# Performance work log

Hardware: AMD Instinct MI355X
Metric: run time of the kernel (lower is better)

Reference implementation:

```python
import jax, jax.numpy as jnp
import numpy as np

NHEAD = 8  # matches init_kwargs

M_NODES = 20000
D_MODEL = 512
N_EDGES = 640000


def setup_inputs() -> dict:
    key = jax.random.key(0)
    ks = jax.random.split(key, 8)
    sc = 1.0 / np.sqrt(D_MODEL)
    return {
        "s": jax.random.normal(ks[0], (M_NODES, D_MODEL), dtype=jnp.float32),
        "edge_index": jax.random.randint(ks[1], (2, N_EDGES), 0, M_NODES, dtype=jnp.int64),
        "Wq": jax.random.normal(ks[2], (D_MODEL, D_MODEL), dtype=jnp.float32) * sc,
        "bq": jax.random.normal(ks[3], (D_MODEL,), dtype=jnp.float32) * sc,
        "Wkv": jax.random.normal(ks[4], (2 * D_MODEL, D_MODEL), dtype=jnp.float32) * sc,
        "bkv": jax.random.normal(ks[5], (2 * D_MODEL,), dtype=jnp.float32) * sc,
        "Wo": jax.random.normal(ks[6], (D_MODEL, D_MODEL), dtype=jnp.float32) * sc,
        "bo": jax.random.normal(ks[7], (D_MODEL,), dtype=jnp.float32) * sc,
    }


def reference(s, edge_index, Wq, bq, Wkv, bkv, Wo, bo):
    M, C = s.shape
    H = NHEAD
    Dh = C // H
    scale = 1.0 / np.sqrt(Dh).astype(np.float32)

    q = (s @ Wq.T + bq).reshape(M, H, Dh)            # [M,H,Dh]
    kv = (s @ Wkv.T + bkv).reshape(M, H, 2 * Dh)     # [M,H,2Dh]
    k, v = kv[..., :Dh], kv[..., Dh:]

    src, tgt = edge_index[0], edge_index[1]

    # per-edge attention logits [E,H]
    a = jnp.einsum('ehc,ehc->eh', q[tgt], k[src]) * scale

    # segment softmax over edges sharing the same target node
    a_max = jax.ops.segment_max(a, tgt, num_segments=M)        # [M,H]
    ex = jnp.exp(a - a_max[tgt])                               # [E,H]
    denom = jax.ops.segment_sum(ex, tgt, num_segments=M)      # [M,H]
    attn = ex / denom[tgt]                                     # [E,H]

    # weighted message aggregation: scatter-sum over target nodes
    o_msg = attn[..., None] * v[src]                           # [E,H,Dh]
    o = jax.ops.segment_sum(o_msg, tgt, num_segments=M)       # [M,H,Dh]
    o = o.reshape(M, C)
    return o @ Wo.T + bo
```

## Files before the change

### kernel.cpp

```cpp
#include <hip/hip_runtime.h>
#include <cmath>

#define MN 20000
#define DM 512
#define NE 640000
#define CAP 128
#define NT 20
#define TSHIFT 10

typedef short  bf16x8 __attribute__((ext_vector_type(8)));
typedef float  f32x4  __attribute__((ext_vector_type(4)));

__device__ __forceinline__ ushort f2b(float x) {
    unsigned u = __builtin_bit_cast(unsigned, x);
    u += 0x7FFF + ((u >> 16) & 1);
    return (ushort)(u >> 16);
}
__device__ __forceinline__ float b2f(ushort b) {
    return __builtin_bit_cast(float, (unsigned)b << 16);
}

#define NS4   (MN * DM / 4)
#define NWC4  (1536 * 512 / 4)
#define NWO4  (512 * 512 / 4)
#define NB4   (1536 / 4)

__device__ __forceinline__ const float* wc_src_row(int r, const float* Wq, const float* Wkv) {
    if (r < 512) return Wq + ((size_t)r << 9);
    if (r < 1024) { int h = (r - 512) >> 6, j = (r - 512) & 63;  return Wkv + ((size_t)(h * 128 + j) << 9); }
    { int h = (r - 1024) >> 6, j = (r - 1024) & 63; return Wkv + ((size_t)(h * 128 + 64 + j) << 9); }
}

__global__ void conv_all_k(const float* __restrict__ s, const float* __restrict__ Wq,
                           const float* __restrict__ Wkv, const float* __restrict__ Wo,
                           const float* __restrict__ bq, const float* __restrict__ bkv,
                           const int* __restrict__ esrc, const int* __restrict__ etgt,
                           int* __restrict__ counts, int* __restrict__ counts2,
                           ushort* __restrict__ s_b, ushort* __restrict__ Wc_b,
                           ushort* __restrict__ Wo_b, float* __restrict__ bc)
{
    int i = blockIdx.x * blockDim.x + threadIdx.x;
    if (i < NE) {
        int t = etgt[i];
        atomicAdd(&counts[t], 1);
        atomicAdd(&counts2[t * NT + (esrc[i] >> TSHIFT)], 1);
    }
    if (i < NS4) {
        float4 v = ((const float4*)s)[i];
        ushort4 o = { f2b(v.x), f2b(v.y), f2b(v.z), f2b(v.w) };
        ((ushort4*)s_b)[i] = o;
        return;
    }
    i -= NS4;
    if (i < NWC4) {
        int e = i * 4, row = e >> 9, col = e & 511;
        float4 v = *(const float4*)(wc_src_row(row, Wq, Wkv) + col);
        ushort4 o = { f2b(v.x), f2b(v.y), f2b(v.z), f2b(v.w) };
        ((ushort4*)Wc_b)[i] = o;
        return;
    }
    i -= NWC4;
    if (i < NWO4) {
        float4 v = ((const float4*)Wo)[i];
        ushort4 o = { f2b(v.x), f2b(v.y), f2b(v.z), f2b(v.w) };
        ((ushort4*)Wo_b)[i] = o;
        return;
    }
    i -= NWO4;
    if (i < NB4) {
#pragma unroll
        for (int u = 0; u < 4; ++u) {
            int r = i * 4 + u;
            float v;
            if (r < 512) v = bq[r];
            else if (r < 1024) { int h = (r - 512) >> 6, j = (r - 512) & 63;  v = bkv[h * 128 + j]; }
            else               { int h = (r - 1024) >> 6, j = (r - 1024) & 63; v = bkv[h * 128 + 64 + j]; }
            bc[r] = v;
        }
    }
}

template<bool OUTBF>
__global__ __launch_bounds__(512) void gemm_mfma(
    const ushort* __restrict__ Ah, const ushort* __restrict__ Bh,
    const float* __restrict__ bias, void* __restrict__ Cout,
    int M, int N, int K, int NCB)
{
    __shared__ ushort lds[2 * 16384];
    const int nwg = gridDim.x;
    const int o = blockIdx.x;
    const int q8 = nwg >> 3, r8 = nwg & 7, x = o & 7, sl = o >> 3;
    const int wg = (x < r8 ? x * (q8 + 1) : r8 * (q8 + 1) + (x - r8) * q8) + sl;
    const int row0 = (wg / NCB) * 256, col0 = (wg % NCB) * 256;

    const int tid = threadIdx.x;
    const int wid = tid >> 6, l = tid & 63;
    const int wm = (wid >> 2) * 128;
    const int wn = (wid & 3) * 64;
    const int fr = l & 15, g = l >> 4;
    const int fcb = g << 4;

    f32x4 acc[8][4] = {};

    for (int k0 = 0; k0 < K; k0 += 64) {
        __syncthreads();
#pragma unroll
        for (int p = 0; p < 4; ++p) {
            const int lb  = p * 8192 + tid * 16;
            const int r   = lb >> 7;
            const int cbs = (lb & 127) ^ ((r & 7) << 4);
            const int ar  = min(row0 + r, M - 1);
            const int br  = col0 + r;
            const size_t aoff = (size_t)ar * K + k0 + (cbs >> 1);
            const size_t boff = (size_t)br * K + k0 + (cbs >> 1);
            __builtin_amdgcn_global_load_lds(
                (const __attribute__((address_space(1))) void*)(Ah + aoff),
                (__attribute__((address_space(3))) void*)&lds[0 * 16384 + (lb >> 1)], 16, 0, 0);
            __builtin_amdgcn_global_load_lds(
                (const __attribute__((address_space(1))) void*)(Bh + boff),
                (__attribute__((address_space(3))) void*)&lds[1 * 16384 + (lb >> 1)], 16, 0, 0);
        }
        __syncthreads();

#pragma unroll
        for (int kk = 0; kk < 2; ++kk) {
            bf16x8 a[8], b[4];
#pragma unroll
            for (int m = 0; m < 8; ++m) {
                const int r  = wm + m * 16 + fr;
                const int cb = (kk * 64 + fcb) ^ ((r & 7) << 4);
                a[m] = *(const bf16x8*)&lds[0 * 16384 + r * 64 + (cb >> 1)];
            }
#pragma unroll
            for (int n = 0; n < 4; ++n) {
                const int r  = wn + n * 16 + fr;
                const int cb = (kk * 64 + fcb) ^ ((r & 7) << 4);
                b[n] = *(const bf16x8*)&lds[1 * 16384 + r * 64 + (cb >> 1)];
            }
#pragma unroll
            for (int m = 0; m < 8; ++m)
#pragma unroll
                for (int n = 0; n < 4; ++n)
                    acc[m][n] = __builtin_amdgcn_mfma_f32_16x16x32_bf16(a[m], b[n], acc[m][n], 0, 0, 0);
        }
    }

#pragma unroll
    for (int n = 0; n < 4; ++n) {
        const int cg = col0 + wn + n * 16 + fr;
        const float bv = bias[cg];
#pragma unroll
        for (int m = 0; m < 8; ++m) {
#pragma unroll
            for (int j = 0; j < 4; ++j) {
                const int rg = row0 + wm + m * 16 + g * 4 + j;
                if (rg < M) {
                    const float v = acc[m][n][j] + bv;
                    if (OUTBF) ((ushort*)Cout)[(size_t)rg * N + cg] = f2b(v);
                    else       ((float*)Cout)[(size_t)rg * N + cg] = v;
                }
            }
        }
    }
}

__global__ __launch_bounds__(1024) void scan_counts_k(
    const int* __restrict__ counts, int* __restrict__ indptr,
    int* __restrict__ dbase, int M)
{
    __shared__ int part[1024];
    __shared__ int hist[128];
    const int t  = threadIdx.x;
    if (t < 128) hist[t] = 0;
    __syncthreads();
    const int CH = (M + 1023) / 1024;
    const int base = t * CH;
    int sum = 0;
    for (int i = 0; i < CH; ++i) {
        int idx = base + i;
        if (idx < M) {
            int c = counts[idx];
            sum += c;
            atomicAdd(&hist[127 - min(c, 127)], 1);
        }
    }
    part[t] = sum;
    __syncthreads();
    for (int off = 1; off < 1024; off <<= 1) {
        int v = (t >= off) ? part[t - off] : 0;
        __syncthreads();
        part[t] += v;
        __syncthreads();
    }
    int excl = part[t] - sum;
    for (int i = 0; i < CH; ++i) {
        int idx = base + i;
        if (idx < M) { indptr[idx] = excl; excl += counts[idx]; }
    }
    if (t == 1023) indptr[M] = part[1023];
    if (t == 0) {
        int run = 0;
        for (int b = 0; b < 128; ++b) { int v = hist[b]; dbase[b] = run; run += v; }
    }
}

__global__ void tileoff_k(const int* __restrict__ indptr, const int* __restrict__ counts2,
                          int* __restrict__ cursor2, int M)
{
    int n = blockIdx.x * blockDim.x + threadIdx.x;
    if (n >= M) return;
    int run = indptr[n];
#pragma unroll
    for (int j = 0; j < NT; ++j) {
        cursor2[n * NT + j] = run;
        run += counts2[n * NT + j];
    }
}

__global__ void scatter_fused_k(const int* __restrict__ src, const int* __restrict__ tgt,
                                int* __restrict__ cursor2, int* __restrict__ slot_off,
                                const int* __restrict__ counts, const int* __restrict__ dbase,
                                int* __restrict__ dcur, int* __restrict__ perm, int E, int M)
{
    int e = blockIdx.x * blockDim.x + threadIdx.x;
    if (e < E) {
        int t = tgt[e], s = src[e];
        int pos = atomicAdd(&cursor2[t * NT + (s >> TSHIFT)], 1);
        slot_off[pos] = s * 3072;
    }
    if (e < M) {
        int b = 127 - min(counts[e], 127);
        int pos = atomicAdd(&dcur[b], 1);
        perm[dbase[b] + pos] = e;
    }
}

__global__ __launch_bounds__(256, 4) void attn11_k(
    const ushort* __restrict__ qkv, const int* __restrict__ indptr,
    const int* __restrict__ slot_off, const int* __restrict__ perm,
    ushort* __restrict__ obh)
{
    __shared__ int slots[4][CAP];
    const int w = threadIdx.x >> 6;
    const int l = threadIdx.x & 63;
    const int node = perm[blockIdx.x * 4 + w];
    const int beg = indptr[node], end = indptr[node + 1];
    const int d = end - beg;
    const int dc = min(d, CAP);

    for (int i = l; i < dc; i += 64) slots[w][i] = slot_off[beg + i];
    __syncthreads();

    const char* base = (const char*)qkv + (l << 4);

    float qf[8];
    {
        bf16x8 qv = *(const bf16x8*)(base + (size_t)node * 3072);
#pragma unroll
        for (int j = 0; j < 8; ++j) qf[j] = b2f((ushort)qv[j]);
    }

    float acc[8] = {};
    float ssum = 0.f;

    int i = 0;
    for (; i + 8 <= dc; i += 8) {
        const int4 sa = *(const int4*)&slots[w][i];
        const int4 sb = *(const int4*)&slots[w][i + 4];
        const char* bp[8] = { base + sa.x, base + sa.y, base + sa.z, base + sa.w,
                              base + sb.x, base + sb.y, base + sb.z, base + sb.w };
        bf16x8 kk[8], vv[8];
#pragma unroll
        for (int u = 0; u < 8; ++u) {
            kk[u] = *(const bf16x8*)(bp[u] + 1024);
            vv[u] = *(const bf16x8*)(bp[u] + 2048);
        }
        float p[8];
#pragma unroll
        for (int u = 0; u < 8; ++u) {
            float pu = 0.f;
#pragma unroll
            for (int j = 0; j < 8; ++j) pu = fmaf(qf[j], b2f((ushort)kk[u][j]), pu);
            p[u] = pu;
        }
#pragma unroll
        for (int u = 0; u < 8; ++u) p[u] += __shfl_xor(p[u], 1);
#pragma unroll
        for (int u = 0; u < 8; ++u) p[u] += __shfl_xor(p[u], 2);
#pragma unroll
        for (int u = 0; u < 8; ++u) p[u] += __shfl_xor(p[u], 4);
        float wt[8];
#pragma unroll
        for (int u = 0; u < 8; ++u) { wt[u] = __expf(p[u] * 0.125f); ssum += wt[u]; }
#pragma unroll
        for (int u = 0; u < 8; ++u)
#pragma unroll
            for (int j = 0; j < 8; ++j) acc[j] = fmaf(wt[u], b2f((ushort)vv[u][j]), acc[j]);
    }
    for (; i < d; ++i) {
        const int so = (i < CAP) ? slots[w][i] : slot_off[beg + i];
        const char* b0 = base + so;
        bf16x8 k0 = *(const bf16x8*)(b0 + 1024);
        bf16x8 v0 = *(const bf16x8*)(b0 + 2048);
        float p0 = 0.f;
#pragma unroll
        for (int j = 0; j < 8; ++j) p0 = fmaf(qf[j], b2f((ushort)k0[j]), p0);
        p0 += __shfl_xor(p0, 1); p0 += __shfl_xor(p0, 2); p0 += __shfl_xor(p0, 4);
        const float w0 = __expf(p0 * 0.125f);
        ssum += w0;
#pragma unroll
        for (int j = 0; j < 8; ++j) acc[j] = fmaf(w0, b2f((ushort)v0[j]), acc[j]);
    }

    const float inv = (d > 0) ? 1.f / ssum : 0.f;
    ushort4 ph0, ph1;
    ph0.x = f2b(acc[0] * inv); ph0.y = f2b(acc[1] * inv);
    ph0.z = f2b(acc[2] * inv); ph0.w = f2b(acc[3] * inv);
    ph1.x = f2b(acc[4] * inv); ph1.y = f2b(acc[5] * inv);
    ph1.z = f2b(acc[6] * inv); ph1.w = f2b(acc[7] * inv);
    const size_t ob_off = (size_t)node * 512 + (l << 3);
    *(ushort4*)(obh + ob_off)     = ph0;
    *(ushort4*)(obh + ob_off + 4) = ph1;
}

extern "C" void kernel_launch(void* const* d_in, const int* in_sizes, int n_in,
                              void* d_out, int out_size, void* d_ws, size_t ws_size,
                              hipStream_t stream)
{
    const float* s   = (const float*)d_in[0];
    const int*   eix = (const int*)d_in[1];
    const float* Wq  = (const float*)d_in[2];
    const float* bq  = (const float*)d_in[3];
    const float* Wkv = (const float*)d_in[4];
    const float* bkv = (const float*)d_in[5];
    const float* Wo  = (const float*)d_in[6];
    const float* bo  = (const float*)d_in[7];
    float* out = (float*)d_out;

    char* ws = (char*)d_ws;
    auto take = [&](size_t bytes) { char* p = ws; ws += (bytes + 255) & ~(size_t)255; return p; };
    ushort* qkv_b  = (ushort*)take((size_t)MN * 1536 * 2);
    ushort* s_b    = (ushort*)take((size_t)MN * 512 * 2);
    ushort* obh    = (ushort*)take((size_t)MN * 512 * 2);
    ushort* Wc_b   = (ushort*)take((size_t)1536 * 512 * 2);
    ushort* Wo_b   = (ushort*)take((size_t)512 * 512 * 2);
    float*  bc     = (float*)take(1536 * 4);
    int* counts    = (int*)take(((size_t)MN + 128 + (size_t)MN * NT) * 4);
    int* dcur      = counts + MN;
    int* counts2   = dcur + 128;
    int* cursor2   = (int*)take((size_t)MN * NT * 4);
    int* slot_off  = (int*)take((size_t)NE * 4);
    int* indptr    = (int*)take((MN + 4) * 4);
    int* dbase     = (int*)take(128 * 4);
    int* perm      = (int*)take(MN * 4);

    hipMemsetAsync(counts, 0, ((size_t)MN + 128 + (size_t)MN * NT) * 4, stream);

    const int convN = NS4 + NWC4 + NWO4 + NB4;
    conv_all_k<<<(convN + 255) / 256, 256, 0, stream>>>(s, Wq, Wkv, Wo, bq, bkv,
                                                        eix, eix + NE, counts, counts2,
                                                        s_b, Wc_b, Wo_b, bc);

    scan_counts_k<<<1, 1024, 0, stream>>>(counts, indptr, dbase, MN);
    tileoff_k<<<(MN + 255) / 256, 256, 0, stream>>>(indptr, counts2, cursor2, MN);
    scatter_fused_k<<<NE / 256, 256, 0, stream>>>(eix, eix + NE, cursor2, slot_off,
                                                  counts, dbase, dcur, perm, NE, MN);

    const int g1 = ((MN + 255) / 256) * (1536 / 256);
    gemm_mfma<true><<<g1, 512, 0, stream>>>(s_b, Wc_b, bc, qkv_b,
                                            MN, 1536, DM, 1536 / 256);

    attn11_k<<<MN / 4, 256, 0, stream>>>(qkv_b, indptr, slot_off, perm, obh);

    const int g2 = ((MN + 255) / 256) * (512 / 256);
    gemm_mfma<false><<<g2, 512, 0, stream>>>(obh, Wo_b, bo, out,
                                             MN, 512, DM, 512 / 256);
}
```

Measured before the change: 402.0 us.

## Double-buffer QKV GEMM LDS loads and use 128-tile output GEMM

The QKV projection GEMM now uses two LDS buffers, issuing global-to-LDS loads for the next K tile while MFMAs run on the current one, with explicit vmcnt waits and barriers. The output projection switches to a separate 128x128-tile kernel with 256 threads, launching more workgroups to fill the GPU better for the narrow N=512 GEMM. Double buffering doubles LDS use to 128KB per block, which may limit occupancy. The smaller tiles trade per-block data reuse for parallelism.

```diff
diff --git a/kernel.cpp b/kernel.cpp
--- a/kernel.cpp
+++ b/kernel.cpp
@@ -80,13 +80,12 @@
     }
 }
 
-template<bool OUTBF>
-__global__ __launch_bounds__(512) void gemm_mfma(
+__global__ __launch_bounds__(512) void gemm_pipe_k(
     const ushort* __restrict__ Ah, const ushort* __restrict__ Bh,
-    const float* __restrict__ bias, void* __restrict__ Cout,
+    const float* __restrict__ bias, ushort* __restrict__ Cout,
     int M, int N, int K, int NCB)
 {
-    __shared__ ushort lds[2 * 16384];
+    __shared__ ushort lds[2][2 * 16384];
     const int nwg = gridDim.x;
     const int o = blockIdx.x;
     const int q8 = nwg >> 3, r8 = nwg & 7, x = o & 7, sl = o >> 3;
@@ -95,15 +94,11 @@
 
     const int tid = threadIdx.x;
     const int wid = tid >> 6, l = tid & 63;
-    const int wm = (wid >> 2) * 128;
-    const int wn = (wid & 3) * 64;
+    const int wm = (wid >> 2) * 128, wn = (wid & 3) * 64;
     const int fr = l & 15, g = l >> 4;
     const int fcb = g << 4;
 
-    f32x4 acc[8][4] = {};
-
-    for (int k0 = 0; k0 < K; k0 += 64) {
-        __syncthreads();
+    auto STAGE = [&](int bi, int k0) {
 #pragma unroll
         for (int p = 0; p < 4; ++p) {
             const int lb  = p * 8192 + tid * 16;
@@ -115,12 +110,28 @@
             const size_t boff = (size_t)br * K + k0 + (cbs >> 1);
             __builtin_amdgcn_global_load_lds(
                 (const __attribute__((address_space(1))) void*)(Ah + aoff),
-                (__attribute__((address_space(3))) void*)&lds[0 * 16384 + (lb >> 1)], 16, 0, 0);
+                (__attribute__((address_space(3))) void*)&lds[bi][0 * 16384 + (lb >> 1)], 16, 0, 0);
             __builtin_amdgcn_global_load_lds(
                 (const __attribute__((address_space(1))) void*)(Bh + boff),
-                (__attribute__((address_space(3))) void*)&lds[1 * 16384 + (lb >> 1)], 16, 0, 0);
-        }
-        __syncthreads();
+                (__attribute__((address_space(3))) void*)&lds[bi][1 * 16384 + (lb >> 1)], 16, 0, 0);
+        }
+    };
+
+    f32x4 acc[8][4] = {};
+    const int NTILES = K >> 6;
+
+    STAGE(0, 0);
+    for (int T = 0; T < NTILES; ++T) {
+        const int cur = T & 1;
+        if (T + 1 < NTILES) {
+            STAGE(cur ^ 1, (T + 1) << 6);
+            asm volatile("s_waitcnt vmcnt(8)" ::: "memory");
+        } else {
+            asm volatile("s_waitcnt vmcnt(0)" ::: "memory");
+        }
+        __builtin_amdgcn_sched_barrier(0);
+        __builtin_amdgcn_s_barrier();
+        __builtin_amdgcn_sched_barrier(0);
 
 #pragma unroll
         for (int kk = 0; kk < 2; ++kk) {
@@ -129,13 +140,13 @@
             for (int m = 0; m < 8; ++m) {
                 const int r  = wm + m * 16 + fr;
                 const int cb = (kk * 64 + fcb) ^ ((r & 7) << 4);
-                a[m] = *(const bf16x8*)&lds[0 * 16384 + r * 64 + (cb >> 1)];
+                a[m] = *(const bf16x8*)&lds[cur][0 * 16384 + r * 64 + (cb >> 1)];
             }
 #pragma unroll
             for (int n = 0; n < 4; ++n) {
                 const int r  = wn + n * 16 + fr;
                 const int cb = (kk * 64 + fcb) ^ ((r & 7) << 4);
-                b[n] = *(const bf16x8*)&lds[1 * 16384 + r * 64 + (cb >> 1)];
+                b[n] = *(const bf16x8*)&lds[cur][1 * 16384 + r * 64 + (cb >> 1)];
             }
 #pragma unroll
             for (int m = 0; m < 8; ++m)
@@ -143,6 +154,9 @@
                 for (int n = 0; n < 4; ++n)
                     acc[m][n] = __builtin_amdgcn_mfma_f32_16x16x32_bf16(a[m], b[n], acc[m][n], 0, 0, 0);
         }
+
+        __builtin_amdgcn_sched_barrier(0);
+        __builtin_amdgcn_s_barrier();
     }
 
 #pragma unroll
@@ -154,11 +168,86 @@
 #pragma unroll
             for (int j = 0; j < 4; ++j) {
                 const int rg = row0 + wm + m * 16 + g * 4 + j;
-                if (rg < M) {
-                    const float v = acc[m][n][j] + bv;
-                    if (OUTBF) ((ushort*)Cout)[(size_t)rg * N + cg] = f2b(v);
-                    else       ((float*)Cout)[(size_t)rg * N + cg] = v;
-                }
+                if (rg < M) Cout[(size_t)rg * N + cg] = f2b(acc[m][n][j] + bv);
+            }
+        }
+    }
+}
+
+__global__ __launch_bounds__(256) void gemm_mfma128(
+    const ushort* __restrict__ Ah, const ushort* __restrict__ Bh,
+    const float* __restrict__ bias, float* __restrict__ Cout,
+    int M, int N, int K, int NCB)
+{
+    constexpr int LDSH = 128 * 64;
+    __shared__ ushort lds[2 * LDSH];
+    const int nwg = gridDim.x;
+    const int o = blockIdx.x;
+    const int q8 = nwg >> 3, r8 = nwg & 7, x = o & 7, sl = o >> 3;
+    const int wg = (x < r8 ? x * (q8 + 1) : r8 * (q8 + 1) + (x - r8) * q8) + sl;
+    const int row0 = (wg / NCB) * 128, col0 = (wg % NCB) * 128;
+
+    const int tid = threadIdx.x;
+    const int wid = tid >> 6, l = tid & 63;
+    const int wm = (wid >> 1) * 64, wn = (wid & 1) * 64;
+    const int fr = l & 15, g = l >> 4;
+    const int fcb = g << 4;
+
+    f32x4 acc[4][4] = {};
+
+    for (int k0 = 0; k0 < K; k0 += 64) {
+        __syncthreads();
+#pragma unroll
+        for (int p = 0; p < 4; ++p) {
+            const int lb  = p * 4096 + tid * 16;
+            const int r   = lb >> 7;
+            const int cbs = (lb & 127) ^ ((r & 7) << 4);
+            const int ar  = min(row0 + r, M - 1);
+            const int br  = col0 + r;
+            const size_t aoff = (size_t)ar * K + k0 + (cbs >> 1);
+            const size_t boff = (size_t)br * K + k0 + (cbs >> 1);
+            __builtin_amdgcn_global_load_lds(
+                (const __attribute__((address_space(1))) void*)(Ah + aoff),
+                (__attribute__((address_space(3))) void*)&lds[0 * LDSH + (lb >> 1)], 16, 0, 0);
+            __builtin_amdgcn_global_load_lds(
+                (const __attribute__((address_space(1))) void*)(Bh + boff),
+                (__attribute__((address_space(3))) void*)&lds[1 * LDSH + (lb >> 1)], 16, 0, 0);
+        }
+        __syncthreads();
+
+#pragma unroll
+        for (int kk = 0; kk < 2; ++kk) {
+            bf16x8 a[4], b[4];
+#pragma unroll
+            for (int m = 0; m < 4; ++m) {
+                const int r  = wm + m * 16 + fr;
+                const int cb = (kk * 64 + fcb) ^ ((r & 7) << 4);
+                a[m] = *(const bf16x8*)&lds[0 * LDSH + r * 64 + (cb >> 1)];
+            }
+#pragma unroll
+            for (int n = 0; n < 4; ++n) {
+                const int r  = wn + n * 16 + fr;
+                const int cb = (kk * 64 + fcb) ^ ((r & 7) << 4);
+                b[n] = *(const bf16x8*)&lds[1 * LDSH + r * 64 + (cb >> 1)];
+            }
+#pragma unroll
+            for (int m = 0; m < 4; ++m)
+#pragma unroll
+                for (int n = 0; n < 4; ++n)
+                    acc[m][n] = __builtin_amdgcn_mfma_f32_16x16x32_bf16(a[m], b[n], acc[m][n], 0, 0, 0);
+        }
+    }
+
+#pragma unroll
+    for (int n = 0; n < 4; ++n) {
+        const int cg = col0 + wn + n * 16 + fr;
+        const float bv = bias[cg];
+#pragma unroll
+        for (int m = 0; m < 4; ++m) {
+#pragma unroll
+            for (int j = 0; j < 4; ++j) {
+                const int rg = row0 + wm + m * 16 + g * 4 + j;
+                if (rg < M) Cout[(size_t)rg * N + cg] = acc[m][n][j] + bv;
             }
         }
     }
@@ -367,12 +456,10 @@
                                                   counts, dbase, dcur, perm, NE, MN);
 
     const int g1 = ((MN + 255) / 256) * (1536 / 256);
-    gemm_mfma<true><<<g1, 512, 0, stream>>>(s_b, Wc_b, bc, qkv_b,
-                                            MN, 1536, DM, 1536 / 256);
+    gemm_pipe_k<<<g1, 512, 0, stream>>>(s_b, Wc_b, bc, qkv_b, MN, 1536, DM, 1536 / 256);
 
     attn11_k<<<MN / 4, 256, 0, stream>>>(qkv_b, indptr, slot_off, perm, obh);
 
-    const int g2 = ((MN + 255) / 256) * (512 / 256);
-    gemm_mfma<false><<<g2, 512, 0, stream>>>(obh, Wo_b, bo, out,
-                                             MN, 512, DM, 512 / 256);
-}
+    const int g2 = ((MN + 127) / 128) * (512 / 128);
+    gemm_mfma128<<<g2, 256, 0, stream>>>(obh, Wo_b, bo, out, MN, 512, DM, 512 / 128);
+}
```

Result: faster. 387.2 us (median of 2 runs) (-3.7%).
